# Kernel optimization log

Measured on AMD Instinct MI355X. Metric: run time of the kernel, lower is better.

Reference implementation:

```python
import jax, jax.numpy as jnp
import numpy as np

N = 4096          # number of real POIs (distance_matrix is [N, N])
D = 64            # poi_dim
B = 8             # users (samples)
DAYS = 4          # days per user
L = 64            # POI ids per day
SCALE = 50.0      # max distance -> arange(0, 50+0.5, 0.5) = 101 bucket boundaries
NUM_INTERVALS = 101


def setup_inputs() -> dict:
    key = jax.random.key(0)
    k1, k2, k3 = jax.random.split(key, 3)
    poi_weight = jax.random.normal(k1, (N + 1, D), dtype=jnp.float32)
    distance_matrix = jax.random.uniform(k2, (N, N), dtype=jnp.float32) * SCALE
    # POI ids in [1, N]: no padding zeros, so lastDay[lastDay != 0] == lastDay (static shape)
    seqInDay = jax.random.randint(k3, (B * DAYS, L), 1, N + 1)
    sampleIdOfDay_set = jnp.repeat(jnp.arange(B), DAYS)
    return {
        "poi_weight": poi_weight,
        "distance_matrix": distance_matrix,
        "seqInDay": seqInDay,
        "sampleIdOfDay_set": sampleIdOfDay_set,
        "GCN_layer_num": 2,
    }


def reference(poi_weight, distance_matrix, seqInDay, sampleIdOfDay_set, GCN_layer_num):
    # group days by sample id (stable sort == torch sorted+groupby); equal group sizes
    ids = np.asarray(sampleIdOfDay_set)
    order = np.argsort(ids, kind="stable")
    nb = int(np.unique(ids).size)
    days = ids.shape[0] // nb
    samples = seqInDay[order].reshape(nb, days, -1)            # [B, days, L]

    poi_emb = poi_weight[1:]                                    # [N, D]
    intervals = jnp.arange(0.0, SCALE + 0.5, 0.5)               # [NUM_INTERVALS]
    # bucket of every distance entry under the torch mask rule:
    # intervals[i-1] <= d < intervals[i]  <=>  searchsorted(side='right')
    dm_bucket = jnp.searchsorted(intervals, distance_matrix, side="right")  # [N, N] int
    diag = jnp.arange(distance_matrix.shape[0])
    scale = jnp.sqrt(jnp.float32(poi_weight.shape[1]))

    def per_sample(sample):                                     # sample: [days, L]
        lastDay = sample[-1]                                    # all ids nonzero
        spans = distance_matrix[lastDay[:-1] - 1, lastDay[1:] - 1]
        # torch.bucketize(right=False) == searchsorted side='left'
        span_idx = jnp.searchsorted(intervals, spans, side="left")
        w = jnp.bincount(span_idx, length=NUM_INTERVALS).astype(jnp.float32)
        w = w / w.sum()
        # buckets actually visited by this sample (torch loops over unique())
        present = jnp.zeros(NUM_INTERVALS, dtype=bool).at[span_idx].set(True)
        W = jnp.where(present[dm_bucket], w[dm_bucket], 0.0)    # [N, N]
        W = W.at[diag, diag].set(1.0)                            # fill_diagonal_(1)
        deg = jnp.maximum(jnp.sqrt(W.sum(-1, keepdims=True)), 1e-12)
        adj = W / deg / deg.T                                    # D^-1/2 A D^-1/2
        out = poi_emb
        layer = poi_emb
        for _ in range(GCN_layer_num):
            layer = jnp.tanh(adj @ layer)
            out = out + layer                                    # sum over stacked layers
        table = jnp.concatenate([poi_weight[:1], out], axis=0)  # [N+1, D]
        return table[sample] * scale                             # [days, L, D]

    res = jax.vmap(per_sample)(samples)                          # [B, days, L, D]
    return res.reshape(nb * days, samples.shape[-1], -1)
```

## Files before the change

### kernel.cpp

```cpp
#include <hip/hip_runtime.h>
#include <hip/hip_bf16.h>
#include <math.h>

typedef __bf16 bf16x8 __attribute__((ext_vector_type(8)));
typedef float  f32x4  __attribute__((ext_vector_type(4)));
typedef unsigned short ushort_t;
typedef unsigned char  u8;
typedef unsigned int   u32;

#define N_POI 4096
#define NB    8
#define NPAIR 4
#define NDAYS 4
#define LSEQ  64
#define NROWS 32
#define NBINS 102
#define KC    6
#define KC2   16
#define NPOS  2048

static __device__ __forceinline__ u32 bf16bits(float f) {
  u32 x = __float_as_uint(f);
  return ((x + 0x7FFFu + ((x >> 16) & 1u)) >> 16) & 0xFFFFu;
}

static __device__ __forceinline__ float lo16f(u32 v) {
  return __uint_as_float(v << 16);
}
static __device__ __forceinline__ float hi16f(u32 v) {
  return __uint_as_float(v & 0xFFFF0000u);
}

static __device__ __forceinline__ void gload16(void* lds, const void* g) {
  __builtin_amdgcn_global_load_lds(
      (const __attribute__((address_space(1))) u32*)g,
      (__attribute__((address_space(3))) u32*)lds, 16, 0, 0);
}

__global__ __launch_bounds__(64) void k_sample(const int* __restrict__ ids,
                                               const int* __restrict__ seq,
                                               const float* __restrict__ dm,
                                               float* __restrict__ tfp,
                                               u32* __restrict__ tbu,
                                               int* __restrict__ meta,
                                               int* __restrict__ rowids) {
  __shared__ int sh_ids[NROWS];
  __shared__ int sh_order[NROWS];
  __shared__ int sh_cnt[NBINS];
  __shared__ int sh_last[LSEQ];
  __shared__ int sh_nb;
  const int tid = threadIdx.x, s = blockIdx.x;
  if (tid < NROWS) sh_ids[tid] = ids[tid];
  for (int k = tid; k < NBINS; k += 64) sh_cnt[k] = 0;
  if (tid == 0) sh_nb = 0;
  __syncthreads();
  if (tid < NROWS) {
    const int my = sh_ids[tid];
    int rank = 0, first = 1;
    for (int j = 0; j < NROWS; ++j) {
      const int v = sh_ids[j];
      if (v < my || (v == my && j < tid)) rank++;
      if (v == my && j < tid) first = 0;
    }
    sh_order[rank] = tid;
    if (first) atomicAdd(&sh_nb, 1);
  }
  __syncthreads();
  const int nb = sh_nb;
  const int days = NROWS / nb;
  if (s == 0) {
    if (tid < NROWS) meta[tid] = sh_order[tid];
    if (tid == 0) meta[NROWS] = days;
  }
  for (int day = 0; day < days; ++day) {
    const int r = s * days + day;
    const int src = sh_order[r];
    rowids[r * LSEQ + tid] = max(seq[src * LSEQ + tid] - 1, 0);
  }
  const int lastRow = sh_order[s * days + days - 1];
  sh_last[tid] = seq[lastRow * LSEQ + tid];
  __syncthreads();
  if (tid < LSEQ - 1) {
    const float v = dm[(size_t)(sh_last[tid] - 1) * N_POI + (sh_last[tid + 1] - 1)];
    int si = (int)ceilf(2.0f * v);
    si = min(max(si, 0), 101);
    atomicAdd(&sh_cnt[si], 1);
  }
  __syncthreads();
  const float inv = 1.0f / (float)(LSEQ - 1);
  for (int k = tid; k < 128; k += 64) {
    const float wv = (k < NBINS) ? (float)sh_cnt[k] * inv : 0.0f;
    tfp[s * 128 + k] = wv;
    tbu[s * 128 + k] = bf16bits(wv);
  }
}

__global__ __launch_bounds__(256) void k_bucket(const float* __restrict__ dm,
                                                const float* __restrict__ tfp,
                                                u8* __restrict__ bucket,
                                                float* __restrict__ rbuf) {
  const int row = blockIdx.x, tid = threadIdx.x;
  __shared__ int h[4][NBINS];
  __shared__ float tl[NB][NBINS];
  __shared__ int sh_bii;
  for (int k = tid; k < 4 * NBINS; k += 256) ((int*)h)[k] = 0;
  __syncthreads();
  const float4* drow = (const float4*)(dm + (size_t)row * N_POI);
  u32* brow = (u32*)(bucket + (size_t)row * N_POI);
  int* hp = h[tid >> 6];
  const int jdiag = row >> 2;
  for (int it = 0; it < 4; ++it) {
    const int j = it * 256 + tid;
    const float4 v = drow[j];
    const int b0 = min((int)(2.0f * v.x) + 1, 101);
    const int b1 = min((int)(2.0f * v.y) + 1, 101);
    const int b2 = min((int)(2.0f * v.z) + 1, 101);
    const int b3 = min((int)(2.0f * v.w) + 1, 101);
    atomicAdd(&hp[b0], 1); atomicAdd(&hp[b1], 1);
    atomicAdd(&hp[b2], 1); atomicAdd(&hp[b3], 1);
    const u32 pk = (u32)b0 | ((u32)b1 << 8) | ((u32)b2 << 16) | ((u32)b3 << 24);
    if (j == jdiag) sh_bii = (int)((pk >> (8 * (row & 3))) & 255u);
    brow[j] = pk;
  }
  for (int idx = tid; idx < NB * NBINS; idx += 256)
    tl[idx / NBINS][idx % NBINS] = tfp[(idx / NBINS) * 128 + (idx % NBINS)];
  __syncthreads();
  for (int k = tid; k < NBINS; k += 256)
    h[0][k] += h[1][k] + h[2][k] + h[3][k];
  __syncthreads();
  const int s = tid >> 5, ln = tid & 31;
  float dot = 0.f;
  for (int k = ln; k < NBINS; k += 32) dot += (float)h[0][k] * tl[s][k];
#pragma unroll
  for (int off = 16; off >= 1; off >>= 1) dot += __shfl_down(dot, off, 32);
  if (ln == 0) {
    const float ri = rsqrtf(dot - tl[s][sh_bii] + 1.0f);
    rbuf[s * N_POI + row] = ri;
  }
}

__global__ __launch_bounds__(256) void k_rows(const float* __restrict__ rbuf,
                                              const float* __restrict__ poi,
                                              ushort_t* __restrict__ y1t) {
  const int s = blockIdx.y;
  const int i = blockIdx.x * 256 + threadIdx.x;
  const float ri = rbuf[s * N_POI + i];
  const float4* prow = (const float4*)(poi + (size_t)(i + 1) * 64);
  ushort_t* dst = y1t + (size_t)s * 64 * N_POI + i;
#pragma unroll
  for (int q = 0; q < 16; ++q) {
    const float4 v = prow[q];
    dst[(size_t)(4 * q + 0) * N_POI] = (ushort_t)bf16bits(ri * v.x);
    dst[(size_t)(4 * q + 1) * N_POI] = (ushort_t)bf16bits(ri * v.y);
    dst[(size_t)(4 * q + 2) * N_POI] = (ushort_t)bf16bits(ri * v.z);
    dst[(size_t)(4 * q + 3) * N_POI] = (ushort_t)bf16bits(ri * v.w);
  }
}

__global__ __launch_bounds__(256, 3) void k_layer(
    const u8* __restrict__ bucket, const u32* __restrict__ tbu,
    const ushort_t* __restrict__ yin, u32* __restrict__ part) {
  const int rb = blockIdx.x, kc = blockIdx.y, g = blockIdx.z;
  const int s0 = 2 * g, s1 = 2 * g + 1;
  const int tid = threadIdx.x;
  const int lane = tid & 63, w = tid >> 6;
  const int loff = tid & 31;

  __shared__ u32 trep[NBINS * 32];
  __shared__ ushort_t Ybuf[2][2][64 * 64];

  const int gi0 = rb * 128;
  const int r0 = gi0 + w * 32 + (lane & 15);
  const u8* brow0 = bucket + (size_t)r0 * N_POI;
  const u8* brow1 = brow0 + (size_t)16 * N_POI;
  const int kq = (lane >> 4) * 8;

  const ushort_t* ybase0 = yin + (size_t)s0 * 64 * N_POI;
  const ushort_t* ybase1 = yin + (size_t)s1 * 64 * N_POI;

  const int d0s = tid >> 3, d1s = 32 + d0s;
  const int bly = (tid & 7) * 16;
  const int sw0 = bly ^ (((d0s & 7) ^ ((d0s >> 3) & 1)) << 4);
  const int sw1 = bly ^ (((d1s & 7) ^ ((d1s >> 3) & 1)) << 4);
  const char* g00 = (const char*)(ybase0 + (size_t)d0s * N_POI) + sw0;
  const char* g01 = (const char*)(ybase0 + (size_t)d1s * N_POI) + sw1;
  const char* g10 = (const char*)(ybase1 + (size_t)d0s * N_POI) + sw0;
  const char* g11 = (const char*)(ybase1 + (size_t)d1s * N_POI) + sw1;

  const int kt0 = (kc * 64) / KC, kt1 = ((kc + 1) * 64) / KC;

  uint2 bpA[4], bpB[4];

#define LOADB_(dst, ktv)                                   \
  {                                                        \
    const int _kb = (ktv) * 64;                            \
    dst[0] = *(const uint2*)(brow0 + _kb + kq);            \
    dst[1] = *(const uint2*)(brow0 + _kb + 32 + kq);       \
    dst[2] = *(const uint2*)(brow1 + _kb + kq);            \
    dst[3] = *(const uint2*)(brow1 + _kb + 32 + kq);       \
  }

#define STAGE_(bufi, ktv)                                  \
  {                                                        \
    const size_t _kb = (size_t)(ktv) * 128;                \
    char* _lb = (char*)&Ybuf[bufi][0][0] + tid * 16;       \
    gload16(_lb, g00 + _kb);                               \
    gload16(_lb + 4096, g01 + _kb);                        \
    gload16(_lb + 8192, g10 + _kb);                        \
    gload16(_lb + 12288, g11 + _kb);                       \
  }

  STAGE_(0, kt0);
  LOADB_(bpA, kt0);
  for (int idx = tid; idx < NBINS * 32; idx += 256) {
    const int b = idx >> 5;
    trep[idx] = tbu[s0 * 128 + b] | (tbu[s1 * 128 + b] << 16);
  }

  f32x4 acc0[2][4], acc1[2][4];
#pragma unroll
  for (int mt = 0; mt < 2; ++mt)
#pragma unroll
    for (int nt = 0; nt < 4; ++nt) {
      acc0[mt][nt] = (f32x4){0.f, 0.f, 0.f, 0.f};
      acc1[mt][nt] = (f32x4){0.f, 0.f, 0.f, 0.f};
    }

  asm volatile("s_waitcnt vmcnt(0)" ::: "memory");
  __syncthreads();

#define BODY_(CB, PB, CUR)                                                     \
  {                                                                            \
    const int k0 = kt * 64;                                                    \
    if (kt + 1 < kt1) { STAGE_((CUR) ^ 1, kt + 1); LOADB_(PB, kt + 1); }       \
    bf16x8 af0[2][2], af1[2][2];                                               \
    _Pragma("unroll") for (int mt = 0; mt < 2; ++mt) {                         \
      _Pragma("unroll") for (int ks = 0; ks < 2; ++ks) {                       \
        const uint2 bb = CB[mt * 2 + ks];                                      \
        u32 tv[8];                                                             \
        _Pragma("unroll") for (int e = 0; e < 4; ++e) tv[e] =                  \
            trep[((bb.x >> (8 * e)) & 255u) * 32 + loff];                      \
        _Pragma("unroll") for (int e = 0; e < 4; ++e) tv[4 + e] =              \
            trep[((bb.y >> (8 * e)) & 255u) * 32 + loff];                      \
        const u32 de = (u32)(r0 + mt * 16 - (k0 + ks * 32 + kq));              \
        if (de < 8u) {             \
          _Pragma("unroll") for (int e = 0; e < 8; ++e)                        \
              if (de == (u32)e) tv[e] = 0x3F803F80u;                           \
        }                                                                      \
        uint4 p0, p1;                                                          \
        p0.x = (tv[0] & 0xFFFFu) | (tv[1] << 16);                              \
        p0.y = (tv[2] & 0xFFFFu) | (tv[3] << 16);                              \
        p0.z = (tv[4] & 0xFFFFu) | (tv[5] << 16);                              \
        p0.w = (tv[6] & 0xFFFFu) | (tv[7] << 16);                              \
        p1.x = (tv[0] >> 16) | (tv[1] & 0xFFFF0000u);                          \
        p1.y = (tv[2] >> 16) | (tv[3] & 0xFFFF0000u);                          \
        p1.z = (tv[4] >> 16) | (tv[5] & 0xFFFF0000u);                          \
        p1.w = (tv[6] >> 16) | (tv[7] & 0xFFFF0000u);                          \
        union { uint4 u; bf16x8 v; } c0, c1;                                   \
        c0.u = p0; c1.u = p1;                                                  \
        af0[mt][ks] = c0.v; af1[mt][ks] = c1.v;                                \
      }                                                                        \
    }                                                                          \
    const char* _y0 = (const char*)&Ybuf[CUR][0][0];                           \
    const char* _y1 = (const char*)&Ybuf[CUR][1][0];                           \
    _Pragma("unroll") for (int ks = 0; ks < 2; ++ks) {                         \
      _Pragma("unroll") for (int nt = 0; nt < 4; ++nt) {                       \
        const int rY = nt * 16 + (lane & 15);                                  \
        const int pm = (rY & 7) ^ ((rY >> 3) & 1);                             \
        const int la = rY * 128 + (((ks * 4 + (lane >> 4)) ^ pm) << 4);        \
        union { uint4 u; bf16x8 v; } b0, b1;                                   \
        b0.u = *(const uint4*)(_y0 + la);                                      \
        b1.u = *(const uint4*)(_y1 + la);                                      \
        acc0[0][nt] = __builtin_amdgcn_mfma_f32_16x16x32_bf16(af0[0][ks], b0.v, \
                                                              acc0[0][nt], 0, 0, 0); \
        acc0[1][nt] = __builtin_amdgcn_mfma_f32_16x16x32_bf16(af0[1][ks], b0.v, \
                                                              acc0[1][nt], 0, 0, 0); \
        acc1[0][nt] = __builtin_amdgcn_mfma_f32_16x16x32_bf16(af1[0][ks], b1.v, \
                                                              acc1[0][nt], 0, 0, 0); \
        acc1[1][nt] = __builtin_amdgcn_mfma_f32_16x16x32_bf16(af1[1][ks], b1.v, \
                                                              acc1[1][nt], 0, 0, 0); \
      }                                                                        \
    }                                                                          \
    asm volatile("s_waitcnt vmcnt(0)" ::: "memory");                           \
    __syncthreads();      \
  }

  int kt = kt0;
  while (true) {
    BODY_(bpA, bpB, 0);
    if (++kt >= kt1) break;
    BODY_(bpB, bpA, 1);
    if (++kt >= kt1) break;
  }

#undef BODY_
#undef STAGE_
#undef LOADB_

#pragma unroll
  for (int mt = 0; mt < 2; ++mt) {
#pragma unroll
    for (int e = 0; e < 4; ++e) {
      const int row = gi0 + w * 32 + mt * 16 + (lane >> 4) * 4 + e;
#pragma unroll
      for (int nt = 0; nt < 4; ++nt) {
        const int col = nt * 16 + (lane & 15);
        part[(((size_t)kc * NPAIR + g) * N_POI + row) * 64 + col] =
            bf16bits(acc0[mt][nt][e]) | (bf16bits(acc1[mt][nt][e]) << 16);
      }
    }
  }
}

__global__ __launch_bounds__(256) void k_reduce(
    const u32* __restrict__ part, const float* __restrict__ rbuf,
    ushort_t* __restrict__ y2t) {
  const int it = blockIdx.x, g = blockIdx.y, tid = threadIdx.x;
  const int s0 = 2 * g, s1 = 2 * g + 1;
  __shared__ ushort_t Tt[2][64 * 72];
#pragma unroll
  for (int j = 0; j < 2; ++j) {
    const int s2 = tid + j * 256;
    const int iloc = s2 >> 3, d0 = (s2 & 7) * 8;
    const int i = it * 64 + iloc;
    const size_t po = ((size_t)g * N_POI + i) * 64 + d0;
    float x0[8] = {0.f, 0.f, 0.f, 0.f, 0.f, 0.f, 0.f, 0.f};
    float x1[8] = {0.f, 0.f, 0.f, 0.f, 0.f, 0.f, 0.f, 0.f};
#pragma unroll
    for (int c = 0; c < KC; ++c) {
      const u32* sp = part + (size_t)c * NPAIR * N_POI * 64;
      uint4 a = *(const uint4*)(sp + po);
      uint4 b = *(const uint4*)(sp + po + 4);
      const u32* au = (const u32*)&a;
      const u32* bu = (const u32*)&b;
#pragma unroll
      for (int q = 0; q < 4; ++q) {
        x0[q] += lo16f(au[q]);     x1[q] += hi16f(au[q]);
        x0[4 + q] += lo16f(bu[q]); x1[4 + q] += hi16f(bu[q]);
      }
    }
    const float r0 = rbuf[s0 * N_POI + i];
    const float r1 = rbuf[s1 * N_POI + i];
#pragma unroll
    for (int e = 0; e < 8; ++e) {
      Tt[0][(d0 + e) * 72 + iloc] = (ushort_t)bf16bits(r0 * tanhf(r0 * x0[e]));
      Tt[1][(d0 + e) * 72 + iloc] = (ushort_t)bf16bits(r1 * tanhf(r1 * x1[e]));
    }
  }
  __syncthreads();
  const int d = tid >> 2, i0 = (tid & 3) * 16;
#pragma unroll
  for (int ps = 0; ps < 2; ++ps) {
    uint4 a = *(const uint4*)&Tt[ps][d * 72 + i0];
    uint4 b = *(const uint4*)&Tt[ps][d * 72 + i0 + 8];
    ushort_t* dst = y2t + ((size_t)(2 * g + ps) * 64 + d) * N_POI + it * 64 + i0;
    *(uint4*)dst = a;
    *(uint4*)(dst + 8) = b;
  }
}

__global__ __launch_bounds__(256) void k_layer2(
    const u8* __restrict__ bucket, const u32* __restrict__ tbu,
    const ushort_t* __restrict__ yin, const int* __restrict__ rowids,
    float* __restrict__ part2) {
  const int rb = blockIdx.x, kc = blockIdx.y;
  const int s = rb >> 1;
  const int tid = threadIdx.x;
  const int lane = tid & 63, w = tid >> 6;
  const int loff = tid & 31;

  __shared__ u32 trep[NBINS * 32];
  __shared__ ushort_t Ybuf[2][64 * 64];

  const int pos0 = rb * 128 + w * 32 + (lane & 15);
  const int rid0 = rowids[pos0];
  const int rid1 = rowids[pos0 + 16];
  const u8* brow0 = bucket + (size_t)rid0 * N_POI;
  const u8* brow1 = bucket + (size_t)rid1 * N_POI;
  const int kq = (lane >> 4) * 8;

  const ushort_t* ybase = yin + (size_t)s * 64 * N_POI;
  const int d0s = tid >> 3, d1s = 32 + d0s;
  const int bly = (tid & 7) * 16;
  const int sw0 = bly ^ (((d0s & 7) ^ ((d0s >> 3) & 1)) << 4);
  const int sw1 = bly ^ (((d1s & 7) ^ ((d1s >> 3) & 1)) << 4);
  const char* gsrc0 = (const char*)(ybase + (size_t)d0s * N_POI) + sw0;
  const char* gsrc1 = (const char*)(ybase + (size_t)d1s * N_POI) + sw1;

  const int kt0 = kc * 4, kt1 = kt0 + 4;

  uint2 bpA[4], bpB[4];

#define LOADB_(dst, ktv)                                   \
  {                                                        \
    const int _kb = (ktv) * 64;                            \
    dst[0] = *(const uint2*)(brow0 + _kb + kq);            \
    dst[1] = *(const uint2*)(brow0 + _kb + 32 + kq);       \
    dst[2] = *(const uint2*)(brow1 + _kb + kq);            \
    dst[3] = *(const uint2*)(brow1 + _kb + 32 + kq);       \
  }

#define STAGE_(bufi, ktv)                                  \
  {                                                        \
    const size_t _kb = (size_t)(ktv) * 128;                \
    char* _lb = (char*)&Ybuf[bufi][0] + tid * 16;          \
    gload16(_lb, gsrc0 + _kb);                             \
    gload16(_lb + 4096, gsrc1 + _kb);                      \
  }

  STAGE_(0, kt0);
  LOADB_(bpA, kt0);
  for (int idx = tid; idx < NBINS * 32; idx += 256)
    trep[idx] = tbu[s * 128 + (idx >> 5)];

  f32x4 acc[2][4];
#pragma unroll
  for (int mt = 0; mt < 2; ++mt)
#pragma unroll
    for (int nt = 0; nt < 4; ++nt) acc[mt][nt] = (f32x4){0.f, 0.f, 0.f, 0.f};

  asm volatile("s_waitcnt vmcnt(0)" ::: "memory");
  __syncthreads();

#define BODY_(CB, PB, CUR)                                                     \
  {                                                                            \
    const int k0 = kt * 64;                                                    \
    if (kt + 1 < kt1) { STAGE_((CUR) ^ 1, kt + 1); LOADB_(PB, kt + 1); }       \
    bf16x8 afr[2][2];                                                          \
    _Pragma("unroll") for (int mt = 0; mt < 2; ++mt) {                         \
      _Pragma("unroll") for (int ks = 0; ks < 2; ++ks) {                       \
        const uint2 bb = CB[mt * 2 + ks];                                      \
        u32 tv[8];                                                             \
        _Pragma("unroll") for (int e = 0; e < 4; ++e) tv[e] =                  \
            trep[((bb.x >> (8 * e)) & 255u) * 32 + loff];                      \
        _Pragma("unroll") for (int e = 0; e < 4; ++e) tv[4 + e] =              \
            trep[((bb.y >> (8 * e)) & 255u) * 32 + loff];                      \
        const int grow = mt ? rid1 : rid0;                                     \
        const u32 de = (u32)(grow - (k0 + ks * 32 + kq));                      \
        if (de < 8u) {                              \
          _Pragma("unroll") for (int e = 0; e < 8; ++e)                        \
              if (de == (u32)e) tv[e] = 0x3F80u;                               \
        }                                                                      \
        uint4 pk;                                                              \
        pk.x = tv[0] | (tv[1] << 16);                                          \
        pk.y = tv[2] | (tv[3] << 16);                                          \
        pk.z = tv[4] | (tv[5] << 16);                                          \
        pk.w = tv[6] | (tv[7] << 16);                                          \
        union { uint4 u; bf16x8 v; } cvt;                                      \
        cvt.u = pk;                                                            \
        afr[mt][ks] = cvt.v;                                                   \
      }                                                                        \
    }                                                                          \
    const char* _yb = (const char*)&Ybuf[CUR][0];                              \
    _Pragma("unroll") for (int ks = 0; ks < 2; ++ks) {                         \
      _Pragma("unroll") for (int nt = 0; nt < 4; ++nt) {                       \
        const int rY = nt * 16 + (lane & 15);                                  \
        const int pm = (rY & 7) ^ ((rY >> 3) & 1);                             \
        const int la = rY * 128 + (((ks * 4 + (lane >> 4)) ^ pm) << 4);        \
        union { uint4 u; bf16x8 v; } bu;                                       \
        bu.u = *(const uint4*)(_yb + la);                                      \
        acc[0][nt] = __builtin_amdgcn_mfma_f32_16x16x32_bf16(afr[0][ks], bu.v, \
                                                             acc[0][nt], 0, 0, 0); \
        acc[1][nt] = __builtin_amdgcn_mfma_f32_16x16x32_bf16(afr[1][ks], bu.v, \
                                                             acc[1][nt], 0, 0, 0); \
      }                                                                        \
    }                                                                          \
    asm volatile("s_waitcnt vmcnt(0)" ::: "memory");                           \
    __syncthreads();                                                           \
  }

  int kt = kt0;
  while (true) {
    BODY_(bpA, bpB, 0);
    if (++kt >= kt1) break;
    BODY_(bpB, bpA, 1);
    if (++kt >= kt1) break;
  }

#undef BODY_
#undef STAGE_
#undef LOADB_

#pragma unroll
  for (int mt = 0; mt < 2; ++mt) {
#pragma unroll
    for (int e = 0; e < 4; ++e) {
      const int pos = rb * 128 + w * 32 + mt * 16 + (lane >> 4) * 4 + e;
#pragma unroll
      for (int nt = 0; nt < 4; ++nt) {
        const int col = nt * 16 + (lane & 15);
        part2[((size_t)kc * NPOS + pos) * 64 + col] = acc[mt][nt][e];
      }
    }
  }
}

__global__ __launch_bounds__(256) void k_gather(const int* __restrict__ seq,
                                                const int* __restrict__ meta,
                                                const float* __restrict__ poi,
                                                const u32* __restrict__ part,
                                                const float* __restrict__ part2,
                                                const float* __restrict__ rbuf,
                                                float* __restrict__ out) {
  const int r = blockIdx.x;
  const int p = blockIdx.y * 4 + (threadIdx.x >> 6);
  const int d = threadIdx.x & 63;
  const int days = meta[NROWS];
  const int srcrow = meta[r];
  const int s = r / days;
  const int id = seq[srcrow * LSEQ + p];
  float v = poi[(size_t)id * 64 + d];
  if (id != 0) {
    const int i = id - 1;
    const size_t po1 = (((size_t)(s >> 1)) * N_POI + i) * 64 + d;
    float x1 = 0.f;
#pragma unroll
    for (int c = 0; c < KC; ++c) {
      const u32 wv = part[(size_t)c * NPAIR * N_POI * 64 + po1];
      x1 += (s & 1) ? hi16f(wv) : lo16f(wv);
    }
    const size_t gq = (size_t)r * LSEQ + p;
    float x2 = 0.f;
#pragma unroll
    for (int c = 0; c < KC2; ++c)
      x2 += part2[((size_t)c * NPOS + gq) * 64 + d];
    const float ri = rbuf[s * N_POI + i];
    v += tanhf(ri * x1) + tanhf(ri * x2);
  }
  out[((size_t)r * LSEQ + p) * 64 + d] = v * 8.0f;
}

extern "C" void kernel_launch(void* const* d_in, const int* in_sizes, int n_in,
                              void* d_out, int out_size, void* d_ws, size_t ws_size,
                              hipStream_t stream) {
  (void)in_sizes; (void)n_in; (void)out_size; (void)ws_size;
  const float* poi = (const float*)d_in[0];
  const float* dm  = (const float*)d_in[1];
  const int*   seq = (const int*)d_in[2];
  const int*   ids = (const int*)d_in[3];

  char* ws = (char*)d_ws;
  size_t off = 0;
  auto carve = [&](size_t bytes) {
    char* p = ws + off;
    off += (bytes + 255) & ~(size_t)255;
    return p;
  };
  u8*       bucket = (u8*)carve((size_t)N_POI * N_POI);
  float*    tfp    = (float*)carve((size_t)NB * 128 * 4);
  u32*      tbu    = (u32*)carve((size_t)NB * 128 * 4);
  float*    rbuf   = (float*)carve((size_t)NB * N_POI * 4);
  ushort_t* y1t    = (ushort_t*)carve((size_t)NB * 64 * N_POI * 2);
  ushort_t* y2t    = (ushort_t*)carve((size_t)NB * 64 * N_POI * 2);
  u32*      part   = (u32*)carve((size_t)KC * NPAIR * N_POI * 64 * 4);
  float*    part2  = (float*)carve((size_t)KC2 * NPOS * 64 * 4);
  int*      rowids = (int*)carve((size_t)NPOS * 4);
  int*      meta   = (int*)carve(256);

  k_sample<<<NB, 64, 0, stream>>>(ids, seq, dm, tfp, tbu, meta, rowids);
  k_bucket<<<N_POI, 256, 0, stream>>>(dm, tfp, bucket, rbuf);
  k_rows<<<dim3(16, NB), 256, 0, stream>>>(rbuf, poi, y1t);
  k_layer<<<dim3(32, KC, NPAIR), 256, 0, stream>>>(bucket, tbu, y1t, part);
  k_reduce<<<dim3(64, NPAIR), 256, 0, stream>>>(part, rbuf, y2t);
  k_layer2<<<dim3(16, KC2), 256, 0, stream>>>(bucket, tbu, y2t, rowids, part2);
  k_gather<<<dim3(NROWS, 16), 256, 0, stream>>>(seq, meta, poi, part, part2, rbuf,
                                                (float*)d_out);
}
```

Baseline: 168.3 us.

## Prefetch bucket tiles two steps ahead with asm loads and split vmcnt waits

```diff
diff --git a/kernel.cpp b/kernel.cpp
--- a/kernel.cpp
+++ b/kernel.cpp
@@ -4,6 +4,7 @@
 
 typedef __bf16 bf16x8 __attribute__((ext_vector_type(8)));
 typedef float  f32x4  __attribute__((ext_vector_type(4)));
+typedef unsigned int u32x2 __attribute__((ext_vector_type(2)));
 typedef unsigned short ushort_t;
 typedef unsigned char  u8;
 typedef unsigned int   u32;
@@ -189,15 +190,19 @@
 
   const int kt0 = (kc * 64) / KC, kt1 = ((kc + 1) * 64) / KC;
 
-  uint2 bpA[4], bpB[4];
-
-#define LOADB_(dst, ktv)                                   \
-  {                                                        \
-    const int _kb = (ktv) * 64;                            \
-    dst[0] = *(const uint2*)(brow0 + _kb + kq);            \
-    dst[1] = *(const uint2*)(brow0 + _kb + 32 + kq);       \
-    dst[2] = *(const uint2*)(brow1 + _kb + kq);            \
-    dst[3] = *(const uint2*)(brow1 + _kb + 32 + kq);       \
+  u32x2 bpA[4], bpB[4];
+
+#define LOADB_ASM(dst, ktv)                                                    \
+  {                                                                            \
+    const int _kb = (ktv) * 64;                                                \
+    asm volatile("global_load_dwordx2 %0, %1, off"                             \
+                 : "=&v"(dst[0]) : "v"(brow0 + _kb + kq));                     \
+    asm volatile("global_load_dwordx2 %0, %1, off"                             \
+                 : "=&v"(dst[1]) : "v"(brow0 + _kb + 32 + kq));                \
+    asm volatile("global_load_dwordx2 %0, %1, off"                             \
+                 : "=&v"(dst[2]) : "v"(brow1 + _kb + kq));                     \
+    asm volatile("global_load_dwordx2 %0, %1, off"                             \
+                 : "=&v"(dst[3]) : "v"(brow1 + _kb + 32 + kq));                \
   }
 
 #define STAGE_(bufi, ktv)                                  \
@@ -211,7 +216,8 @@
   }
 
   STAGE_(0, kt0);
-  LOADB_(bpA, kt0);
+  LOADB_ASM(bpA, kt0);
+  LOADB_ASM(bpB, kt0 + 1);
   for (int idx = tid; idx < NBINS * 32; idx += 256) {
     const int b = idx >> 5;
     trep[idx] = tbu[s0 * 128 + b] | (tbu[s1 * 128 + b] << 16);
@@ -226,22 +232,24 @@
       acc1[mt][nt] = (f32x4){0.f, 0.f, 0.f, 0.f};
     }
 
-  asm volatile("s_waitcnt vmcnt(0)" ::: "memory");
-  __syncthreads();
-
-#define BODY_(CB, PB, CUR)                                                     \
+  __syncthreads();
+
+#define BODY_(CB, CUR)                                                         \
   {                                                                            \
+                 \
+    if (kt + 1 < kt1) asm volatile("s_waitcnt vmcnt(8)" ::: "memory");         \
+    else              asm volatile("s_waitcnt vmcnt(4)" ::: "memory");         \
+    __builtin_amdgcn_sched_barrier(0);     \
     const int k0 = kt * 64;                                                    \
-    if (kt + 1 < kt1) { STAGE_((CUR) ^ 1, kt + 1); LOADB_(PB, kt + 1); }       \
     bf16x8 af0[2][2], af1[2][2];                                               \
     _Pragma("unroll") for (int mt = 0; mt < 2; ++mt) {                         \
       _Pragma("unroll") for (int ks = 0; ks < 2; ++ks) {                       \
-        const uint2 bb = CB[mt * 2 + ks];                                      \
+        const u32x2 bb = CB[mt * 2 + ks];                                      \
         u32 tv[8];                                                             \
         _Pragma("unroll") for (int e = 0; e < 4; ++e) tv[e] =                  \
-            trep[((bb.x >> (8 * e)) & 255u) * 32 + loff];                      \
+            trep[((bb[0] >> (8 * e)) & 255u) * 32 + loff];                     \
         _Pragma("unroll") for (int e = 0; e < 4; ++e) tv[4 + e] =              \
-            trep[((bb.y >> (8 * e)) & 255u) * 32 + loff];                      \
+            trep[((bb[1] >> (8 * e)) & 255u) * 32 + loff];                     \
         const u32 de = (u32)(r0 + mt * 16 - (k0 + ks * 32 + kq));              \
         if (de < 8u) {             \
           _Pragma("unroll") for (int e = 0; e < 8; ++e)                        \
@@ -261,6 +269,11 @@
         af0[mt][ks] = c0.v; af1[mt][ks] = c1.v;                                \
       }                                                                        \
     }                                                                          \
+           \
+    if (kt + 1 < kt1) asm volatile("s_waitcnt vmcnt(4)" ::: "memory");         \
+    else              asm volatile("s_waitcnt vmcnt(0)" ::: "memory");         \
+    __builtin_amdgcn_s_barrier();                                              \
+    __builtin_amdgcn_sched_barrier(0);      \
     const char* _y0 = (const char*)&Ybuf[CUR][0][0];                           \
     const char* _y1 = (const char*)&Ybuf[CUR][1][0];                           \
     _Pragma("unroll") for (int ks = 0; ks < 2; ++ks) {                         \
@@ -281,21 +294,23 @@
                                                               acc1[1][nt], 0, 0, 0); \
       }                                                                        \
     }                                                                          \
-    asm volatile("s_waitcnt vmcnt(0)" ::: "memory");                           \
-    __syncthreads();      \
+      \
+    if (kt + 1 < kt1) { STAGE_((CUR) ^ 1, kt + 1); }                           \
+    __builtin_amdgcn_sched_barrier(0);          \
+    if (kt + 2 < kt1) { LOADB_ASM(CB, kt + 2); }                               \
   }
 
   int kt = kt0;
   while (true) {
-    BODY_(bpA, bpB, 0);
+    BODY_(bpA, 0);
     if (++kt >= kt1) break;
-    BODY_(bpB, bpA, 1);
+    BODY_(bpB, 1);
     if (++kt >= kt1) break;
   }
 
 #undef BODY_
 #undef STAGE_
-#undef LOADB_
+#undef LOADB_ASM
 
 #pragma unroll
   for (int mt = 0; mt < 2; ++mt) {
```

Result: no change. 167.9 us (-0.2%).
